# Optimization experiments

Measured on AMD Instinct MI355X. Metric: run time of the kernel, lower is better.

Reference implementation:

```python
import jax, jax.numpy as jnp
import numpy as np

N = 50000
F_IN = 512
H1, C1 = 8, 16          # layer-1 heads / per-head channels
H2, C2 = 1, 40          # layer-2 heads / num_classes
NEG_SLOPE = 0.2


def setup_inputs() -> dict:
    key = jax.random.key(0)
    ks = jax.random.split(key, 10)
    E = 800000
    x = jax.random.normal(ks[0], (N, F_IN), dtype=jnp.float32)
    edge_index = jax.random.randint(ks[1], (2, E), 0, N, dtype=jnp.int64)
    s1 = 1.0 / np.sqrt(F_IN)
    s2 = 1.0 / np.sqrt(H1 * C1)
    return {
        "x": x,
        "edge_index": edge_index,
        "W1": jax.random.normal(ks[2], (F_IN, H1 * C1), dtype=jnp.float32) * s1,
        "att_src1": jax.random.normal(ks[3], (H1, C1), dtype=jnp.float32) * s2,
        "att_dst1": jax.random.normal(ks[4], (H1, C1), dtype=jnp.float32) * s2,
        "b1": jnp.zeros((H1 * C1,), dtype=jnp.float32),
        "W2": jax.random.normal(ks[5], (H1 * C1, H2 * C2), dtype=jnp.float32) * s2,
        "att_src2": jax.random.normal(ks[6], (H2, C2), dtype=jnp.float32) * (1.0 / np.sqrt(C2)),
        "att_dst2": jax.random.normal(ks[7], (H2, C2), dtype=jnp.float32) * (1.0 / np.sqrt(C2)),
        "b2": jnp.zeros((H2 * C2,), dtype=jnp.float32),
    }


def _gat_conv(x, W, att_src, att_dst, b, src, dst, H, C):
    # x: [N, Fin] -> h: [N, H, C]
    h = (x @ W).reshape(N, H, C)
    a_src = jnp.einsum("nhc,hc->nh", h, att_src)  # [N, H]
    a_dst = jnp.einsum("nhc,hc->nh", h, att_dst)
    e = a_src[src] + a_dst[dst]                    # [E, H]
    e = jax.nn.leaky_relu(e, NEG_SLOPE)
    # segment softmax over edges sharing the same target node (dst)
    m = jax.ops.segment_max(e, dst, num_segments=N)         # [N, H]
    ex = jnp.exp(e - m[dst])
    denom = jax.ops.segment_sum(ex, dst, num_segments=N)    # [N, H]
    alpha = ex / (denom[dst] + 1e-16)                        # [E, H]
    msg = h[src] * alpha[..., None]                          # [E, H, C]
    out = jax.ops.segment_sum(msg, dst, num_segments=N)     # [N, H, C]
    return out.reshape(N, H * C) + b


def reference(x, edge_index, W1, att_src1, att_dst1, b1, W2, att_src2, att_dst2, b2):
    # add self-loops (PyG GATConv default)
    loop = jnp.arange(N, dtype=edge_index.dtype)
    src = jnp.concatenate([edge_index[0], loop])
    dst = jnp.concatenate([edge_index[1], loop])
    h = _gat_conv(x, W1, att_src1, att_dst1, b1, src, dst, H1, C1)
    h = jax.nn.elu(h)
    h = _gat_conv(h, W2, att_src2, att_dst2, b2, src, dst, H2, C2)
    return jax.nn.log_softmax(h, axis=1)
```

## Files before the change

### kernel.cpp

```cpp
#include <hip/hip_runtime.h>
#include <math.h>

#define N_NODES 50000
#define FIN 512
#define NE 800000
#define ETOT 850000
#define F1 128
#define H1 8
#define F2 40
#define BCAP 64
#define NBIN 196
#define BINCAP 6144

typedef __attribute__((ext_vector_type(8))) short bf16x8;
typedef __attribute__((ext_vector_type(4))) float f32x4;

__device__ inline ushort f2bf(float f){
  union{float f; unsigned u;} v; v.f=f;
  return (ushort)((v.u + 0x8000u) >> 16);
}
__device__ inline float bflo(uint u){ union{uint a;float f;} v; v.a = u << 16;         return v.f; }
__device__ inline float bfhi(uint u){ union{uint a;float f;} v; v.a = u & 0xffff0000u; return v.f; }
__device__ inline float bf1(ushort u){ union{uint a;float f;} v; v.a = ((uint)u) << 16; return v.f; }

__device__ inline bf16x8 cvt8(float4 a, float4 b){
  union{ushort u[8]; bf16x8 v;} r;
  r.u[0]=f2bf(a.x); r.u[1]=f2bf(a.y); r.u[2]=f2bf(a.z); r.u[3]=f2bf(a.w);
  r.u[4]=f2bf(b.x); r.u[5]=f2bf(b.y); r.u[6]=f2bf(b.z); r.u[7]=f2bf(b.w);
  return r.v;
}


__global__ __launch_bounds__(1024) void k_pro(const int* __restrict__ src, const int* __restrict__ dst,
                                              int* __restrict__ binCursor, uint* __restrict__ binbuf,
                                              const float* __restrict__ W1, const float* __restrict__ W2,
                                              ushort* __restrict__ Wtb, ushort* __restrict__ Wt2){
  __shared__ int hist[256];
  __shared__ int base[256];
  int bx = blockIdx.x, t = threadIdx.x;

  if(bx < 104){
    if(t < 256) hist[t] = 0;
    __syncthreads();

    uint pk[8]; int bn[8];
    int i0 = bx*8192 + t;
    #pragma unroll
    for(int k=0;k<8;k++){
      int i = i0 + k*1024;
      int d = -1, s = 0;
      if(i < NE){ d = dst[i]; s = src[i]; }
      else if(i < ETOT){ d = i - NE; s = d; }
      if(d >= 0){
        bn[k] = d >> 8;
        pk[k] = ((uint)d << 16) | (uint)s;
        atomicAdd(&hist[bn[k]], 1);
      } else bn[k] = -1;
    }
    __syncthreads();
    if(t < 256){
      int h = hist[t];
      base[t] = (t < NBIN && h > 0) ? atomicAdd(&binCursor[t], h) : 0;
    }
    __syncthreads();
    if(t < 256) hist[t] = 0;
    __syncthreads();
    #pragma unroll
    for(int k=0;k<8;k++){
      if(bn[k] >= 0){
        int off = atomicAdd(&hist[bn[k]], 1);
        binbuf[(size_t)bn[k]*BINCAP + base[bn[k]] + off] = pk[k];
      }
    }
  } else {
    int id = (bx - 104)*1024 + t;
    if(id < 65536){
      int k = id >> 7, n = id & 127;
      Wtb[(size_t)(k>>3)*1024 + n*8 + (k&7)] = f2bf(W1[id]);
    } else {
      int id2 = id - 65536;
      if(id2 < 6144){
        int j = id2 & 7;
        int tt = id2 >> 3;
        int n = tt % 48;
        int t2 = tt / 48;
        int quad = t2 & 3, ks = t2 >> 2;
        int k = ks*32 + quad*8 + j;
        Wt2[id2] = (n < F2) ? f2bf(W2[k*F2 + n]) : (ushort)0;
      }
    }
  }
}


__global__ __launch_bounds__(1024) void k_g1b(const int* __restrict__ binCursor, const uint* __restrict__ binbuf,
                                              int* __restrict__ cnt, ushort* __restrict__ bucket,
                                              const float* __restrict__ x, const ushort* __restrict__ Wtb,
                                              const float* __restrict__ as_w, const float* __restrict__ ad_w,
                                              ushort* __restrict__ h1b,
                                              float* __restrict__ a_src, float* __restrict__ a_dst){
  __shared__ int lcnt[256];
  __shared__ ushort lb[256][BCAP];
  __shared__ ushort Asm[4][2][32][72];
  int bxg = blockIdx.x;

  if(bxg < NBIN){
    int b = bxg, t = threadIdx.x;
    if(t < 256) lcnt[t] = 0;
    __syncthreads();
    int m = min(binCursor[b], BINCAP);
    const uint* p = binbuf + (size_t)b*BINCAP;
    for(int i=t; i<m; i+=1024){
      uint pk = p[i];
      int dl = (pk >> 16) & 255;
      int pos = atomicAdd(&lcnt[dl], 1);
      if(pos < BCAP) lb[dl][pos] = (ushort)(pk & 0xFFFF);
    }
    __syncthreads();
    int n0 = b << 8;
    int nrows = min(256, N_NODES - n0);
    if(t < nrows) cnt[n0 + t] = lcnt[t];
    const uint4* s4 = (const uint4*)lb;
    uint4* d4 = (uint4*)(bucket + (size_t)n0*BCAP);
    int total = nrows * 8;
    for(int i=t; i<total; i+=1024) d4[i] = s4[i];
    return;
  }

  int sub = threadIdx.x >> 8;
  int tid = threadIdx.x & 255;
  int tileIdx = (bxg - NBIN)*4 + sub;
  int bx = min(tileIdx, 1562);

  int wave = tid >> 6, lane = tid & 63;
  int l15 = lane & 15, quad = lane >> 4;

  f32x4 acc[2][2];
  #pragma unroll
  for(int i=0;i<2;i++)
    #pragma unroll
    for(int j=0;j<2;j++) acc[i][j] = (f32x4){0.f,0.f,0.f,0.f};

  int am  = tid >> 3;
  int ak8 = (tid & 7) << 3;
  int agr = bx*32 + am;
  int agrc = min(agr, N_NODES-1);
  const float* xrow = x + (size_t)agrc*FIN + ak8;

  {
    float4 a0 = *(const float4*)xrow;
    float4 a1 = *(const float4*)(xrow + 4);
    *(bf16x8*)&Asm[sub][0][am][ak8] = cvt8(a0, a1);
  }

  const ushort* wpB = Wtb + (size_t)quad*1024 + (size_t)(wave*32 + l15)*8;

  bf16x8 bcur[2][2];
  #pragma unroll
  for(int ks=0;ks<2;ks++)
    #pragma unroll
    for(int tn=0;tn<2;tn++)
      bcur[ks][tn] = *(const bf16x8*)(wpB + ks*4096 + tn*128);
  __syncthreads();

  for(int kt=0; kt<FIN; kt+=64){
    int cur = (kt >> 6) & 1;
    bool hn = (kt + 64) < FIN;

    float4 a0, a1;
    if(hn){
      a0 = *(const float4*)(xrow + kt + 64);
      a1 = *(const float4*)(xrow + kt + 68);
    }
    bf16x8 bnext[2][2];
    if(hn){
      #pragma unroll
      for(int ks=0;ks<2;ks++)
        #pragma unroll
        for(int tn=0;tn<2;tn++)
          bnext[ks][tn] = *(const bf16x8*)(wpB + (size_t)(kt+64)*128 + ks*4096 + tn*128);
    }

    bf16x8 af[2][2];
    #pragma unroll
    for(int tm=0;tm<2;tm++)
      #pragma unroll
      for(int ks=0;ks<2;ks++)
        af[tm][ks] = *(bf16x8*)&Asm[sub][cur][tm*16 + l15][ks*32 + quad*8];

    #pragma unroll
    for(int ks=0;ks<2;ks++)
      #pragma unroll
      for(int tm=0;tm<2;tm++)
        #pragma unroll
        for(int tn=0;tn<2;tn++)
          acc[tm][tn] = __builtin_amdgcn_mfma_f32_16x16x32_bf16(af[tm][ks], bcur[ks][tn], acc[tm][tn], 0,0,0);

    if(hn)
      *(bf16x8*)&Asm[sub][cur^1][am][ak8] = cvt8(a0, a1);
    __syncthreads();
    #pragma unroll
    for(int ks=0;ks<2;ks++)
      #pragma unroll
      for(int tn=0;tn<2;tn++)
        bcur[ks][tn] = bnext[ks][tn];
  }

  float wsv[2], wdv[2];
  #pragma unroll
  for(int tn=0;tn<2;tn++){
    int h = wave*2 + tn;
    wsv[tn] = as_w[h*16 + l15];
    wdv[tn] = ad_w[h*16 + l15];
  }

  #pragma unroll
  for(int tm=0;tm<2;tm++){
    #pragma unroll
    for(int r=0;r<4;r++){
      int row = bx*32 + tm*16 + quad*4 + r;
      bool ok = row < N_NODES;
      #pragma unroll
      for(int tn=0;tn<2;tn++){
        float v = acc[tm][tn][r];
        if(ok){
          int col = wave*32 + tn*16 + l15;
          h1b[(size_t)row*F1 + col] = f2bf(v);
        }
        float ss = v * wsv[tn];
        float dd = v * wdv[tn];
        #pragma unroll
        for(int m=8;m;m>>=1){ ss += __shfl_xor(ss, m); dd += __shfl_xor(dd, m); }
        if(ok && l15 == 0){
          int h = wave*2 + tn;
          a_src[(size_t)row*H1 + h] = ss;
          a_dst[(size_t)row*H1 + h] = dd;
        }
      }
    }
  }
}


__global__ __launch_bounds__(256) void k_agg1(const ushort* __restrict__ h1b, const float* __restrict__ a_src,
                                              const float* __restrict__ a_dst,
                                              const int* __restrict__ cnt, const ushort* __restrict__ bucket,
                                              const float* __restrict__ b1, ushort* __restrict__ gb){
  int wave = threadIdx.x >> 6, lane = threadIdx.x & 63;
  int n = blockIdx.x*4 + wave;
  if(n >= N_NODES) return;
  int hl = lane >> 3;
  float adv = a_dst[n*H1 + hl];
  int deg = min(cnt[n], BCAP);
  int sv = (int)bucket[(n << 6) + lane];
  const uint* h1u = (const uint*)h1b;

  float ws0=0.f, ax0=0.f, ay0=0.f;
  float ws1=0.f, ax1=0.f, ay1=0.f;
  float ws2=0.f, ax2=0.f, ay2=0.f;
  float ws3=0.f, ax3=0.f, ay3=0.f;
  int j = 0;
  for(; j+3<deg; j+=4){
    int s0 = __shfl(sv, j),   s1 = __shfl(sv, j+1);
    int s2 = __shfl(sv, j+2), s3 = __shfl(sv, j+3);
    float e0 = a_src[s0*H1 + hl] + adv;
    float e1 = a_src[s1*H1 + hl] + adv;
    float e2 = a_src[s2*H1 + hl] + adv;
    float e3 = a_src[s3*H1 + hl] + adv;
    e0 = e0 > 0.f ? e0 : 0.2f*e0;  e1 = e1 > 0.f ? e1 : 0.2f*e1;
    e2 = e2 > 0.f ? e2 : 0.2f*e2;  e3 = e3 > 0.f ? e3 : 0.2f*e3;
    float w0=__expf(e0), w1=__expf(e1), w2=__expf(e2), w3=__expf(e3);
    uint u0 = h1u[(size_t)s0*64 + lane];
    uint u1 = h1u[(size_t)s1*64 + lane];
    uint u2 = h1u[(size_t)s2*64 + lane];
    uint u3 = h1u[(size_t)s3*64 + lane];
    ax0 += w0*bflo(u0); ay0 += w0*bfhi(u0); ws0 += w0;
    ax1 += w1*bflo(u1); ay1 += w1*bfhi(u1); ws1 += w1;
    ax2 += w2*bflo(u2); ay2 += w2*bfhi(u2); ws2 += w2;
    ax3 += w3*bflo(u3); ay3 += w3*bfhi(u3); ws3 += w3;
  }
  for(; j<deg; j++){
    int s0 = __shfl(sv, j);
    float e0 = a_src[s0*H1 + hl] + adv;
    e0 = e0 > 0.f ? e0 : 0.2f*e0;
    float w0 = __expf(e0);
    uint u0 = h1u[(size_t)s0*64 + lane];
    ax0 += w0*bflo(u0); ay0 += w0*bfhi(u0); ws0 += w0;
  }
  float wsum = (ws0+ws1)+(ws2+ws3);
  float inv = 1.f/(wsum + 1e-16f);
  int c0 = lane*2;
  float o0 = ((ax0+ax1)+(ax2+ax3))*inv + b1[c0];
  float o1 = ((ay0+ay1)+(ay2+ay3))*inv + b1[c0+1];
  o0 = o0 > 0.f ? o0 : expm1f(o0);
  o1 = o1 > 0.f ? o1 : expm1f(o1);
  uint up = (uint)f2bf(o0) | ((uint)f2bf(o1) << 16);
  ((uint*)gb)[(size_t)n*64 + lane] = up;
}


__global__ __launch_bounds__(256) void k_gemm2(const ushort* __restrict__ gb, const ushort* __restrict__ Wt2,
                                               const float* __restrict__ as_w, const float* __restrict__ ad_w,
                                               ushort* __restrict__ h2b,
                                               float* __restrict__ a_src, float* __restrict__ a_dst){
  int tid = threadIdx.x;
  int wave = tid >> 6, lane = tid & 63;
  int l15 = lane & 15, quad = lane >> 4;
  int row0 = blockIdx.x*64 + wave*16;
  int arow = min(row0 + l15, N_NODES-1);
  const ushort* ap = gb + (size_t)arow*F1 + quad*8;

  f32x4 acc[3];
  #pragma unroll
  for(int tn=0;tn<3;tn++) acc[tn] = (f32x4){0.f,0.f,0.f,0.f};

  #pragma unroll
  for(int ks=0;ks<4;ks++){
    bf16x8 af = *(const bf16x8*)(ap + ks*32);
    #pragma unroll
    for(int tn=0;tn<3;tn++){
      bf16x8 bf = *(const bf16x8*)(Wt2 + ((size_t)(ks*4+quad)*48 + tn*16 + l15)*8);
      acc[tn] = __builtin_amdgcn_mfma_f32_16x16x32_bf16(af, bf, acc[tn], 0,0,0);
    }
  }

  float ws2v[3], wd2v[3];
  #pragma unroll
  for(int tn=0;tn<3;tn++){
    int col = tn*16 + l15;
    ws2v[tn] = (col < F2) ? as_w[col] : 0.f;
    wd2v[tn] = (col < F2) ? ad_w[col] : 0.f;
  }

  #pragma unroll
  for(int r=0;r<4;r++){
    int row = row0 + quad*4 + r;
    bool ok = row < N_NODES;
    float ss = 0.f, dd = 0.f;
    #pragma unroll
    for(int tn=0;tn<3;tn++){
      float v = acc[tn][r];
      int col = tn*16 + l15;
      if(ok && col < F2) h2b[(size_t)row*F2 + col] = f2bf(v);
      ss += v * ws2v[tn];
      dd += v * wd2v[tn];
    }
    #pragma unroll
    for(int m=8;m;m>>=1){ ss += __shfl_xor(ss, m); dd += __shfl_xor(dd, m); }
    if(ok && l15 == 0){
      a_src[row] = ss;
      a_dst[row] = dd;
    }
  }
}


__global__ __launch_bounds__(256) void k_agg2(const ushort* __restrict__ h2b, const float* __restrict__ a_src,
                                              const float* __restrict__ a_dst,
                                              const int* __restrict__ cnt, const ushort* __restrict__ bucket,
                                              const float* __restrict__ b2, float* __restrict__ out){
  int wave = threadIdx.x >> 6, lane = threadIdx.x & 63;
  int n = blockIdx.x*4 + wave;
  if(n >= N_NODES) return;
  float adv = a_dst[n];
  int deg = min(cnt[n], BCAP);
  int sv = (int)bucket[(n << 6) + lane];
  int c = (lane < F2) ? lane : (F2-1);

  float ws0=0.f, ac0=0.f, ws1=0.f, ac1=0.f, ws2=0.f, ac2=0.f, ws3=0.f, ac3=0.f;
  int j = 0;
  for(; j+3<deg; j+=4){
    int s0 = __shfl(sv, j),   s1 = __shfl(sv, j+1);
    int s2 = __shfl(sv, j+2), s3 = __shfl(sv, j+3);
    float e0 = a_src[s0] + adv, e1 = a_src[s1] + adv;
    float e2 = a_src[s2] + adv, e3 = a_src[s3] + adv;
    e0 = e0 > 0.f ? e0 : 0.2f*e0;  e1 = e1 > 0.f ? e1 : 0.2f*e1;
    e2 = e2 > 0.f ? e2 : 0.2f*e2;  e3 = e3 > 0.f ? e3 : 0.2f*e3;
    float w0=__expf(e0), w1=__expf(e1), w2=__expf(e2), w3=__expf(e3);
    ac0 += w0*bf1(h2b[(size_t)s0*F2 + c]); ws0 += w0;
    ac1 += w1*bf1(h2b[(size_t)s1*F2 + c]); ws1 += w1;
    ac2 += w2*bf1(h2b[(size_t)s2*F2 + c]); ws2 += w2;
    ac3 += w3*bf1(h2b[(size_t)s3*F2 + c]); ws3 += w3;
  }
  for(; j<deg; j++){
    int s0 = __shfl(sv, j);
    float e0 = a_src[s0] + adv;
    e0 = e0 > 0.f ? e0 : 0.2f*e0;
    float w0 = __expf(e0);
    ac0 += w0*bf1(h2b[(size_t)s0*F2 + c]); ws0 += w0;
  }
  float v = ((ac0+ac1)+(ac2+ac3))/(((ws0+ws1)+(ws2+ws3)) + 1e-16f) + b2[c];
  float mv = (lane < F2) ? v : -INFINITY;
  #pragma unroll
  for(int off=32; off; off>>=1) mv = fmaxf(mv, __shfl_xor(mv, off));
  float ex = (lane < F2) ? __expf(v - mv) : 0.f;
  #pragma unroll
  for(int off=32; off; off>>=1) ex += __shfl_xor(ex, off);
  if(lane < F2) out[(size_t)n*F2 + lane] = v - mv - logf(ex);
}


extern "C" void kernel_launch(void* const* d_in, const int* in_sizes, int n_in,
                              void* d_out, int out_size, void* d_ws, size_t ws_size,
                              hipStream_t stream) {
  const float* x        = (const float*)d_in[0];
  const int*   eidx     = (const int*)d_in[1];
  const float* W1       = (const float*)d_in[2];
  const float* att_src1 = (const float*)d_in[3];
  const float* att_dst1 = (const float*)d_in[4];
  const float* b1       = (const float*)d_in[5];
  const float* W2       = (const float*)d_in[6];
  const float* att_src2 = (const float*)d_in[7];
  const float* att_dst2 = (const float*)d_in[8];
  const float* b2       = (const float*)d_in[9];
  float* out = (float*)d_out;

  const int* src = eidx;
  const int* dst = eidx + NE;

  ushort* h1b  = (ushort*)d_ws;
  ushort* h2b  = h1b + 6400000;
  ushort* gb   = h2b + 2000000;
  ushort* Wtb  = gb + 6400000;
  ushort* bucket = Wtb + 65536;
  float* a_src1 = (float*)(bucket + 3200000);
  float* a_dst1 = a_src1 + 400000;
  float* a_src2 = a_dst1 + 400000;
  float* a_dst2 = a_src2 + 50000;
  int* cnt      = (int*)(a_dst2 + 50000);
  int* binCursor= cnt + 50002;
  uint* binbuf  = (uint*)(binCursor + 256);
  ushort* Wt2   = (ushort*)(binbuf + (size_t)NBIN*BINCAP);

  hipMemsetAsync(binCursor, 0, NBIN*sizeof(int), stream);

  k_pro<<<174, 1024, 0, stream>>>(src, dst, binCursor, binbuf, W1, W2, Wtb, Wt2);

  k_g1b<<<NBIN + 391, 1024, 0, stream>>>(binCursor, binbuf, cnt, bucket,
                                         x, Wtb, att_src1, att_dst1, h1b, a_src1, a_dst1);

  k_agg1<<<(N_NODES+3)/4, 256, 0, stream>>>(h1b, a_src1, a_dst1, cnt, bucket, b1, gb);

  k_gemm2<<<(N_NODES+63)/64, 256, 0, stream>>>(gb, Wt2, att_src2, att_dst2, h2b, a_src2, a_dst2);
  k_agg2 <<<(N_NODES+3)/4, 256, 0, stream>>>(h2b, a_src2, a_dst2, cnt, bucket, b2, out);
}
```

Measured before the change: 285.5 us.

## Halve bin size and use 256-thread blocks for fused bucketing/GEMM1 kernel

Destination bins shrink from 256 to 128 nodes (391 bins, half capacity each), and the fused bucket-build/GEMM1 kernel moves from 1024-thread blocks holding four GEMM tiles to 256-thread blocks with one tile each, sharing a single small shared-memory buffer. The smaller footprint and finer blocks are meant to raise occupancy and balance load across CUs, and the bucket staging rows are padded to avoid LDS bank conflicts. In exchange there are more blocks, more global atomics on bin cursors, and 32-bit instead of 128-bit stores when copying buckets out. A tighter per-bin capacity also raises the risk of overflow if a bin gets more edges than expected.

```diff
diff --git a/kernel.cpp b/kernel.cpp
--- a/kernel.cpp
+++ b/kernel.cpp
@@ -9,8 +9,8 @@
 #define H1 8
 #define F2 40
 #define BCAP 64
-#define NBIN 196
-#define BINCAP 6144
+#define NBIN 391
+#define BINCAP 3072
 
 typedef __attribute__((ext_vector_type(8))) short bf16x8;
 typedef __attribute__((ext_vector_type(4))) float f32x4;
@@ -35,12 +35,12 @@
                                               int* __restrict__ binCursor, uint* __restrict__ binbuf,
                                               const float* __restrict__ W1, const float* __restrict__ W2,
                                               ushort* __restrict__ Wtb, ushort* __restrict__ Wt2){
-  __shared__ int hist[256];
-  __shared__ int base[256];
+  __shared__ int hist[512];
+  __shared__ int base[512];
   int bx = blockIdx.x, t = threadIdx.x;
 
   if(bx < 104){
-    if(t < 256) hist[t] = 0;
+    if(t < 512) hist[t] = 0;
     __syncthreads();
 
     uint pk[8]; int bn[8];
@@ -52,18 +52,18 @@
       if(i < NE){ d = dst[i]; s = src[i]; }
       else if(i < ETOT){ d = i - NE; s = d; }
       if(d >= 0){
-        bn[k] = d >> 8;
+        bn[k] = d >> 7;
         pk[k] = ((uint)d << 16) | (uint)s;
         atomicAdd(&hist[bn[k]], 1);
       } else bn[k] = -1;
     }
     __syncthreads();
-    if(t < 256){
+    if(t < 512){
       int h = hist[t];
       base[t] = (t < NBIN && h > 0) ? atomicAdd(&binCursor[t], h) : 0;
     }
     __syncthreads();
-    if(t < 256) hist[t] = 0;
+    if(t < 512) hist[t] = 0;
     __syncthreads();
     #pragma unroll
     for(int k=0;k<8;k++){
@@ -93,45 +93,46 @@
 }
 
 
-__global__ __launch_bounds__(1024) void k_g1b(const int* __restrict__ binCursor, const uint* __restrict__ binbuf,
-                                              int* __restrict__ cnt, ushort* __restrict__ bucket,
-                                              const float* __restrict__ x, const ushort* __restrict__ Wtb,
-                                              const float* __restrict__ as_w, const float* __restrict__ ad_w,
-                                              ushort* __restrict__ h1b,
-                                              float* __restrict__ a_src, float* __restrict__ a_dst){
-  __shared__ int lcnt[256];
-  __shared__ ushort lb[256][BCAP];
-  __shared__ ushort Asm[4][2][32][72];
+__global__ __launch_bounds__(256) void k_g1b(const int* __restrict__ binCursor, const uint* __restrict__ binbuf,
+                                             int* __restrict__ cnt, ushort* __restrict__ bucket,
+                                             const float* __restrict__ x, const ushort* __restrict__ Wtb,
+                                             const float* __restrict__ as_w, const float* __restrict__ ad_w,
+                                             ushort* __restrict__ h1b,
+                                             float* __restrict__ a_src, float* __restrict__ a_dst){
+  __shared__ __align__(16) char smem[17408];
   int bxg = blockIdx.x;
 
   if(bxg < NBIN){
+    int* lcnt  = (int*)smem;
+    ushort* lb = (ushort*)(smem + 512);
     int b = bxg, t = threadIdx.x;
-    if(t < 256) lcnt[t] = 0;
+    if(t < 128) lcnt[t] = 0;
     __syncthreads();
     int m = min(binCursor[b], BINCAP);
     const uint* p = binbuf + (size_t)b*BINCAP;
-    for(int i=t; i<m; i+=1024){
+    for(int i=t; i<m; i+=256){
       uint pk = p[i];
-      int dl = (pk >> 16) & 255;
+      int dl = (pk >> 16) & 127;
       int pos = atomicAdd(&lcnt[dl], 1);
-      if(pos < BCAP) lb[dl][pos] = (ushort)(pk & 0xFFFF);
-    }
-    __syncthreads();
-    int n0 = b << 8;
-    int nrows = min(256, N_NODES - n0);
+      if(pos < BCAP) lb[dl*66 + pos] = (ushort)(pk & 0xFFFF);
+    }
+    __syncthreads();
+    int n0 = b << 7;
+    int nrows = min(128, N_NODES - n0);
     if(t < nrows) cnt[n0 + t] = lcnt[t];
-    const uint4* s4 = (const uint4*)lb;
-    uint4* d4 = (uint4*)(bucket + (size_t)n0*BCAP);
-    int total = nrows * 8;
-    for(int i=t; i<total; i+=1024) d4[i] = s4[i];
+    const uint* s4 = (const uint*)(smem + 512);
+    uint* d4 = (uint*)(bucket + ((size_t)n0 << 6));
+    int total = nrows * 32;
+    for(int i=t; i<total; i+=256){
+      int r = i >> 5, c = i & 31;
+      d4[i] = s4[r*33 + c];
+    }
     return;
   }
 
-  int sub = threadIdx.x >> 8;
-  int tid = threadIdx.x & 255;
-  int tileIdx = (bxg - NBIN)*4 + sub;
-  int bx = min(tileIdx, 1562);
-
+  ushort* Asm = (ushort*)smem;
+  int tid = threadIdx.x;
+  int bx  = bxg - NBIN;
   int wave = tid >> 6, lane = tid & 63;
   int l15 = lane & 15, quad = lane >> 4;
 
@@ -150,7 +151,7 @@
   {
     float4 a0 = *(const float4*)xrow;
     float4 a1 = *(const float4*)(xrow + 4);
-    *(bf16x8*)&Asm[sub][0][am][ak8] = cvt8(a0, a1);
+    *(bf16x8*)&Asm[am*72 + ak8] = cvt8(a0, a1);
   }
 
   const ushort* wpB = Wtb + (size_t)quad*1024 + (size_t)(wave*32 + l15)*8;
@@ -186,7 +187,7 @@
     for(int tm=0;tm<2;tm++)
       #pragma unroll
       for(int ks=0;ks<2;ks++)
-        af[tm][ks] = *(bf16x8*)&Asm[sub][cur][tm*16 + l15][ks*32 + quad*8];
+        af[tm][ks] = *(bf16x8*)&Asm[cur*2304 + (tm*16 + l15)*72 + ks*32 + quad*8];
 
     #pragma unroll
     for(int ks=0;ks<2;ks++)
@@ -197,7 +198,7 @@
           acc[tm][tn] = __builtin_amdgcn_mfma_f32_16x16x32_bf16(af[tm][ks], bcur[ks][tn], acc[tm][tn], 0,0,0);
 
     if(hn)
-      *(bf16x8*)&Asm[sub][cur^1][am][ak8] = cvt8(a0, a1);
+      *(bf16x8*)&Asm[(cur^1)*2304 + am*72 + ak8] = cvt8(a0, a1);
     __syncthreads();
     #pragma unroll
     for(int ks=0;ks<2;ks++)
@@ -429,14 +430,14 @@
   float* a_dst2 = a_src2 + 50000;
   int* cnt      = (int*)(a_dst2 + 50000);
   int* binCursor= cnt + 50002;
-  uint* binbuf  = (uint*)(binCursor + 256);
+  uint* binbuf  = (uint*)(binCursor + 512);
   ushort* Wt2   = (ushort*)(binbuf + (size_t)NBIN*BINCAP);
 
-  hipMemsetAsync(binCursor, 0, NBIN*sizeof(int), stream);
+  hipMemsetAsync(binCursor, 0, 512*sizeof(int), stream);
 
   k_pro<<<174, 1024, 0, stream>>>(src, dst, binCursor, binbuf, W1, W2, Wtb, Wt2);
 
-  k_g1b<<<NBIN + 391, 1024, 0, stream>>>(binCursor, binbuf, cnt, bucket,
+  k_g1b<<<NBIN + 1563, 256, 0, stream>>>(binCursor, binbuf, cnt, bucket,
                                          x, Wtb, att_src1, att_dst1, h1b, a_src1, a_dst1);
 
   k_agg1<<<(N_NODES+3)/4, 256, 0, stream>>>(h1b, a_src1, a_dst1, cnt, bucket, b1, gb);
```

Result: no change. 281.7 us (-1.3%).
